# Kernel optimization log

Hardware: AMD Instinct MI355X
Metric: run time of the kernel (lower is better)

## Reference

```python
import jax, jax.numpy as jnp
import numpy as np

EPS = 1e-7          # keras.backend.epsilon()
L2_EPS = 1e-12      # tf.math.l2_normalize epsilon


def _l2_normalize(v):
    # tf.math.l2_normalize: v * rsqrt(max(sum(v^2), 1e-12))
    sq = jnp.sum(v * v, axis=-1, keepdims=True)
    return v * jax.lax.rsqrt(jnp.maximum(sq, L2_EPS))


def setup_inputs() -> dict:
    key = jax.random.key(0)
    k1, k2 = jax.random.split(key)
    x = jax.random.normal(k1, (4, 2048, 1024), dtype=jnp.float32)
    ref = jax.random.normal(k2, (8192, 1024), dtype=jnp.float32)
    return {"x": x, "ref": ref}


def reference(x, ref):
    # inputs += K.epsilon()
    xn = _l2_normalize(x + EPS)          # [B, N, D]
    refn = _l2_normalize(ref)            # [M, D]
    # fused form of sum(xn[..., N, 1, D] * refn[1, M, D], axis=-1) -> [B, N, M]
    return jnp.einsum('bnd,md->bnm', xn, refn)
```

## Files before the change

### kernel.cpp

```cpp
#include <hip/hip_runtime.h>
#include <hip/hip_bf16.h>
#include <stdint.h>

typedef __bf16 bf16x8 __attribute__((ext_vector_type(8)));
typedef float f32x4 __attribute__((ext_vector_type(4)));

#define GLB_AS __attribute__((address_space(1)))
#define LDS_AS __attribute__((address_space(3)))

__device__ __forceinline__ void gload_lds16(const void* g, void* l) {
    __builtin_amdgcn_global_load_lds((GLB_AS void*)(g), (LDS_AS void*)(l), 16, 0, 0);
}

#define GM 8192
#define GN 8192
#define GK 1024
#define NT (GK / 64)
#define NI (NT / 2)

__global__ __launch_bounds__(256) void normalize_rows(
    const float* __restrict__ x, const float* __restrict__ ref,
    __bf16* __restrict__ outA, __bf16* __restrict__ outB)
{
    const int row = blockIdx.x;
    const bool isX = row < 8192;
    const size_t r = isX ? (size_t)row : (size_t)(row - 8192);
    const float* src = isX ? (x + r * 1024) : (ref + r * 1024);
    __bf16* dst = isX ? (outA + r * 1024) : (outB + r * 1024);
    const float eps = isX ? 1e-7f : 0.0f;

    const int t = threadIdx.x;
    float4 v = reinterpret_cast<const float4*>(src)[t];
    v.x += eps; v.y += eps; v.z += eps; v.w += eps;
    float ss = v.x * v.x + v.y * v.y + v.z * v.z + v.w * v.w;

    #pragma unroll
    for (int o = 32; o; o >>= 1) ss += __shfl_xor(ss, o, 64);

    __shared__ float red[4];
    const int wv = t >> 6, lane = t & 63;
    if (lane == 0) red[wv] = ss;
    __syncthreads();
    const float tot = red[0] + red[1] + red[2] + red[3];
    const float inv = rsqrtf(fmaxf(tot, 1e-12f));

    __bf16 b[4];
    b[0] = (__bf16)(v.x * inv);
    b[1] = (__bf16)(v.y * inv);
    b[2] = (__bf16)(v.z * inv);
    b[3] = (__bf16)(v.w * inv);
    uint2 pk;
    __builtin_memcpy(&pk, b, 8);
    reinterpret_cast<uint2*>(dst)[t] = pk;
}

__global__ __launch_bounds__(512, 2) void gemm_bt8(
    const __bf16* __restrict__ A, const __bf16* __restrict__ B,
    float* __restrict__ C)
{
    __shared__ __bf16 As[2][2][128][64];
    __shared__ __bf16 Bs[2][2][128][64];

    const int bid = blockIdx.x;
    const int swz = (bid & 7) * 128 + (bid >> 3);
    const int within = swz & 15;
    const int super  = swz >> 4;
    const int tm = (super & 7) * 4 + (within & 3);
    const int tn = (super >> 3) * 4 + (within >> 2);
    const size_t rowM0 = (size_t)tm * 256;
    const size_t rowN0 = (size_t)tn * 256;

    const int tid  = threadIdx.x;
    const int wave = tid >> 6;
    const int lane = tid & 63;
    const int wr = wave >> 2;
    const int wc = wave & 3;

    const int srow  = lane >> 3;
    const int sslot = (lane & 7) ^ srow;
    const int fr = lane & 15;
    const int fs = lane >> 4;

    bf16x8 af[4][2];
    bf16x8 bq[2][2][2];
    f32x4  acc[8][4] = {};

#define STAGE_A(T, h, b) { \
    _Pragma("unroll") \
    for (int j = 0; j < 2; ++j) { \
        const size_t grow = rowM0 + (size_t)(j) * 128 + (h) * 64 + wave * 8 + srow; \
        const char* src = (const char*)A + (grow * GK + (size_t)(T) * 64) * 2 + sslot * 16; \
        char* dst = (char*)&As[b][h][0][0] + (j * 64 + wave * 8) * 128; \
        gload_lds16(src, dst); } }

#define STAGE_B(T, h, b) { \
    _Pragma("unroll") \
    for (int j = 0; j < 2; ++j) { \
        const int l = j * 64 + wave * 8 + srow; \
        const size_t grow = rowN0 + (size_t)(l >> 5) * 64 + (h) * 32 + (l & 31); \
        const char* src = (const char*)B + (grow * GK + (size_t)(T) * 64) * 2 + sslot * 16; \
        char* dst = (char*)&Bs[b][h][0][0] + (j * 64 + wave * 8) * 128; \
        gload_lds16(src, dst); } }

#define LDA(qm, b) { \
    _Pragma("unroll") \
    for (int m = 0; m < 4; ++m) { \
        const int l = wr * 64 + m * 16 + fr; \
        _Pragma("unroll") \
        for (int ks = 0; ks < 2; ++ks) { \
            const int slot = (ks * 4 + fs) ^ (l & 7); \
            af[m][ks] = *(const bf16x8*)((const char*)&As[b][qm][0][0] + l * 128 + slot * 16); } } }

#define LDB(qn, b) { \
    _Pragma("unroll") \
    for (int n = 0; n < 2; ++n) { \
        const int l = wc * 32 + n * 16 + fr; \
        _Pragma("unroll") \
        for (int ks = 0; ks < 2; ++ks) { \
            const int slot = (ks * 4 + fs) ^ (l & 7); \
            bq[qn][n][ks] = *(const bf16x8*)((const char*)&Bs[b][qn][0][0] + l * 128 + slot * 16); } } }

#define QMFMA(qm, qn) { \
    __builtin_amdgcn_s_setprio(1); \
    _Pragma("unroll") \
    for (int ks = 0; ks < 2; ++ks) \
    _Pragma("unroll") \
    for (int m = 0; m < 4; ++m) \
    _Pragma("unroll") \
    for (int n = 0; n < 2; ++n) \
        acc[(qm) * 4 + m][(qn) * 2 + n] = __builtin_amdgcn_mfma_f32_16x16x32_bf16( \
            af[m][ks], bq[qn][n][ks], acc[(qm) * 4 + m][(qn) * 2 + n], 0, 0, 0); \
    __builtin_amdgcn_s_setprio(0); }

#define BAR() __builtin_amdgcn_s_barrier()
#define WAIT_LGKM0() { asm volatile("s_waitcnt lgkmcnt(0)" ::: "memory"); __builtin_amdgcn_sched_barrier(0); }
#define WAIT_VM(n)   { asm volatile("s_waitcnt vmcnt(" #n ")" ::: "memory"); __builtin_amdgcn_sched_barrier(0); }

    STAGE_A(0, 0, 0); STAGE_A(0, 1, 0); STAGE_B(0, 0, 0); STAGE_B(0, 1, 0);
    STAGE_A(1, 0, 1); STAGE_B(1, 0, 1); STAGE_B(1, 1, 1);
    WAIT_VM(6);
    BAR();

    #pragma unroll 1
    for (int i = 0; i < NI; ++i) {
        const int t1 = 2 * i + 1, t2 = 2 * i + 2, t3 = 2 * i + 3;
        const bool more = (i < NI - 1);

        LDA(0, 0); LDB(0, 0);
        STAGE_A(t1, 1, 1);
        BAR(); WAIT_LGKM0();
        QMFMA(0, 0);
        BAR();
        LDB(1, 0);
        if (more) STAGE_A(t2, 0, 0);
        BAR(); WAIT_LGKM0();
        QMFMA(0, 1);
        BAR();
        LDA(1, 0);
        if (more) STAGE_B(t2, 0, 0);
        BAR(); WAIT_LGKM0();
        QMFMA(1, 0);
        BAR();
        if (more) { STAGE_B(t2, 1, 0); WAIT_VM(6); }
        else      { WAIT_VM(0); }
        BAR();
        QMFMA(1, 1);
        BAR();
        LDA(0, 1); LDB(0, 1);
        if (more) STAGE_A(t2, 1, 0);
        BAR(); WAIT_LGKM0();
        QMFMA(0, 0);
        BAR();
        LDB(1, 1);
        if (more) STAGE_A(t3, 0, 1);
        BAR(); WAIT_LGKM0();
        QMFMA(0, 1);
        BAR();
        LDA(1, 1);
        if (more) STAGE_B(t3, 0, 1);
        BAR(); WAIT_LGKM0();
        QMFMA(1, 0);
        BAR();
        if (more) { STAGE_B(t3, 1, 1); WAIT_VM(6); }
        else      { WAIT_VM(0); }
        BAR();
        QMFMA(1, 1);
        BAR();
    }

    const size_t crow0 = rowM0 + (size_t)wr * 128;
    const size_t ccol0 = rowN0 + (size_t)wc * 64;
    #pragma unroll
    for (int mi = 0; mi < 8; ++mi) {
        #pragma unroll
        for (int ni = 0; ni < 4; ++ni) {
            const size_t col = ccol0 + ni * 16 + (lane & 15);
            const size_t rb  = crow0 + mi * 16 + (lane >> 4) * 4;
            #pragma unroll
            for (int j = 0; j < 4; ++j)
                C[(rb + j) * (size_t)GN + col] = acc[mi][ni][j];
        }
    }

#undef STAGE_A
#undef STAGE_B
#undef LDA
#undef LDB
#undef QMFMA
#undef BAR
#undef WAIT_LGKM0
#undef WAIT_VM
}

__global__ __launch_bounds__(256) void naive_pairwise(
    const float* __restrict__ x, const float* __restrict__ ref,
    float* __restrict__ out)
{
    const int row = blockIdx.x >> 5;
    const int j = (blockIdx.x & 31) * 256 + threadIdx.x;
    const float* xr = x + (size_t)row * 1024;
    const float* rr = ref + (size_t)j * 1024;

    __shared__ float xs[1024];
    float part = 0.f;
    for (int k = threadIdx.x; k < 1024; k += 256) {
        float v = xr[k] + 1e-7f;
        xs[k] = v;
        part += v * v;
    }
    #pragma unroll
    for (int o = 32; o; o >>= 1) part += __shfl_xor(part, o, 64);
    __shared__ float red[4];
    if ((threadIdx.x & 63) == 0) red[threadIdx.x >> 6] = part;
    __syncthreads();
    const float ssx = red[0] + red[1] + red[2] + red[3];

    float ssr = 0.f, dot = 0.f;
    for (int k = 0; k < 1024; ++k) {
        float r = rr[k];
        ssr += r * r;
        dot += r * xs[k];
    }
    out[(size_t)row * 8192 + j] =
        dot * rsqrtf(fmaxf(ssx, 1e-12f)) * rsqrtf(fmaxf(ssr, 1e-12f));
}

extern "C" void kernel_launch(void* const* d_in, const int* in_sizes, int n_in,
                              void* d_out, int out_size, void* d_ws, size_t ws_size,
                              hipStream_t stream) {
    const float* x   = (const float*)d_in[0];
    const float* ref = (const float*)d_in[1];
    float* out = (float*)d_out;

    const size_t need = (size_t)GM * GK * sizeof(__bf16) * 2;
    if (ws_size >= need) {
        __bf16* wsA = (__bf16*)d_ws;
        __bf16* wsB = wsA + (size_t)GM * GK;
        normalize_rows<<<16384, 256, 0, stream>>>(x, ref, wsA, wsB);
        gemm_bt8<<<(GM / 256) * (GN / 256), 512, 0, stream>>>(wsA, wsB, out);
    } else {
        naive_pairwise<<<8192 * 32, 256, 0, stream>>>(x, ref, out);
    }
}
```

Before: 177.7 us.

## Swap MFMA operands for vectorized C stores, overlap epilogue stores, remap tile order

```diff
diff --git a/kernel.cpp b/kernel.cpp
--- a/kernel.cpp
+++ b/kernel.cpp
@@ -62,11 +62,11 @@
     __shared__ __bf16 Bs[2][2][128][64];
 
     const int bid = blockIdx.x;
-    const int swz = (bid & 7) * 128 + (bid >> 3);
-    const int within = swz & 15;
-    const int super  = swz >> 4;
-    const int tm = (super & 7) * 4 + (within & 3);
-    const int tn = (super >> 3) * 4 + (within >> 2);
+    const int g  = bid >> 8;
+    const int x  = bid & 7;
+    const int ii = (bid >> 3) & 31;
+    const int tm = (g & 1) * 16 + (x & 3) * 4 + (ii & 3);
+    const int tn = (g >> 1) * 16 + (x >> 2) * 8 + (ii >> 2);
     const size_t rowM0 = (size_t)tm * 256;
     const size_t rowN0 = (size_t)tn * 256;
 
@@ -129,8 +129,17 @@
     _Pragma("unroll") \
     for (int n = 0; n < 2; ++n) \
         acc[(qm) * 4 + m][(qn) * 2 + n] = __builtin_amdgcn_mfma_f32_16x16x32_bf16( \
-            af[m][ks], bq[qn][n][ks], acc[(qm) * 4 + m][(qn) * 2 + n], 0, 0, 0); \
+            bq[qn][n][ks], af[m][ks], acc[(qm) * 4 + m][(qn) * 2 + n], 0, 0, 0); \
     __builtin_amdgcn_s_setprio(0); }
+
+#define STORE_QUAD(qm, qn) { \
+    _Pragma("unroll") \
+    for (int m = 0; m < 4; ++m) \
+    _Pragma("unroll") \
+    for (int n = 0; n < 2; ++n) { \
+        const size_t row = rowM0 + (size_t)wr * 128 + (qm) * 64 + m * 16 + (lane & 15); \
+        const size_t col = rowN0 + (size_t)wc * 64 + (qn) * 32 + n * 16 + (lane >> 4) * 4; \
+        *reinterpret_cast<f32x4*>(&C[row * (size_t)GN + col]) = acc[(qm) * 4 + m][(qn) * 2 + n]; } }
 
 #define BAR() __builtin_amdgcn_s_barrier()
 #define WAIT_LGKM0() { asm volatile("s_waitcnt lgkmcnt(0)" ::: "memory"); __builtin_amdgcn_sched_barrier(0); }
@@ -170,35 +179,29 @@
         if (more) STAGE_A(t2, 1, 0);
         BAR(); WAIT_LGKM0();
         QMFMA(0, 0);
+        if (!more) STORE_QUAD(0, 0);
         BAR();
         LDB(1, 1);
         if (more) STAGE_A(t3, 0, 1);
         BAR(); WAIT_LGKM0();
         QMFMA(0, 1);
+        if (!more) STORE_QUAD(0, 1);
         BAR();
         LDA(1, 1);
         if (more) STAGE_B(t3, 0, 1);
         BAR(); WAIT_LGKM0();
         QMFMA(1, 0);
-        BAR();
-        if (more) { STAGE_B(t3, 1, 1); WAIT_VM(6); }
-        else      { WAIT_VM(0); }
-        BAR();
-        QMFMA(1, 1);
-        BAR();
-    }
-
-    const size_t crow0 = rowM0 + (size_t)wr * 128;
-    const size_t ccol0 = rowN0 + (size_t)wc * 64;
-    #pragma unroll
-    for (int mi = 0; mi < 8; ++mi) {
-        #pragma unroll
-        for (int ni = 0; ni < 4; ++ni) {
-            const size_t col = ccol0 + ni * 16 + (lane & 15);
-            const size_t rb  = crow0 + mi * 16 + (lane >> 4) * 4;
-            #pragma unroll
-            for (int j = 0; j < 4; ++j)
-                C[(rb + j) * (size_t)GN + col] = acc[mi][ni][j];
+        if (!more) STORE_QUAD(1, 0);
+        BAR();
+        if (more) {
+            STAGE_B(t3, 1, 1); WAIT_VM(6);
+            BAR();
+            QMFMA(1, 1);
+            BAR();
+        } else {
+            BAR();
+            QMFMA(1, 1);
+            STORE_QUAD(1, 1);
         }
     }
 
@@ -207,6 +210,7 @@
 #undef LDA
 #undef LDB
 #undef QMFMA
+#undef STORE_QUAD
 #undef BAR
 #undef WAIT_LGKM0
 #undef WAIT_VM
```

Result: no change. 179.8 us (+1.2%).
